# Optimization experiments

Measured on AMD Instinct MI355X. Metric: run time of the kernel, lower is better.

## Reference

```python
import jax, jax.numpy as jnp
import numpy as np
import math

SUB_LEN = 5

def _row_mask(index, sub_len, win_len):
    # Faithful port of logsparseAttention.row_mask (numpy, built at trace time).
    log_l = math.ceil(math.log2(sub_len))
    mask = np.zeros(win_len, dtype=np.float32)
    if (win_len // sub_len) * 2 * log_l > index:
        mask[: index + 1] = 1.0
    else:
        while index >= 0:
            if index - log_l + 1 < 0:
                mask[:index] = 1.0
                break
            mask[index - log_l + 1 : index + 1] = 1.0
            for i in range(log_l):
                new_index = index - log_l + 1 - 2 ** i
                if index - new_index <= sub_len and new_index >= 0:
                    mask[new_index] = 1.0
            index -= sub_len
    return mask

def _log_mask(win_len, sub_len):
    m = np.stack([_row_mask(i, sub_len, win_len) for i in range(win_len)])
    return m[None, None]  # [1, 1, L, L]

def setup_inputs() -> dict:
    key = jax.random.key(0)
    kq, kk, kv = jax.random.split(key, 3)
    B, L, H, D = 4, 2048, 16, 64
    return {
        "queries": jax.random.normal(kq, (B, L, H, D), dtype=jnp.float32),
        "keys": jax.random.normal(kk, (B, L, H, D), dtype=jnp.float32),
        "values": jax.random.normal(kv, (B, L, H, D), dtype=jnp.float32),
        "attn_mask": jnp.zeros((1,), dtype=jnp.int32),  # unused by the module
    }

def reference(queries, keys, values, attn_mask):
    L = queries.shape[1]
    mask = jnp.asarray(_log_mask(L, SUB_LEN), dtype=queries.dtype)  # [1,1,L,L]
    q = jnp.swapaxes(queries, 1, 2)            # [B, H, L, D]
    k = jnp.transpose(keys, (0, 2, 3, 1))      # [B, H, D, L]
    v = jnp.swapaxes(values, 1, 2)             # [B, H, L, D]
    pre_att = jnp.matmul(q, k)                 # [B, H, L, L] (no scaling: scale=None)
    pre_att = pre_att * mask + (-1e9) * (1.0 - mask)
    att = jax.nn.softmax(pre_att, axis=-1)
    return jnp.matmul(att, v)                  # [B, H, L, D]
```

## Files before the change

### kernel.cpp

```cpp
#include <hip/hip_runtime.h>


typedef __attribute__((ext_vector_type(8))) short short8;
typedef __attribute__((ext_vector_type(4))) float floatx4;
typedef __attribute__((ext_vector_type(16))) float floatx16;
typedef _Float16 half8 __attribute__((ext_vector_type(8)));
typedef _Float16 half4 __attribute__((ext_vector_type(4)));

#define NB 4
#define NL 2048
#define NH 16
#define ND 64
#define PADK 72
#define LOG2E 1.44269504088896340736f

#define KSW(row, col8) (((row) << 6) + ((col8) ^ (((row) & 7) << 3)))

static __device__ __forceinline__ unsigned short f2bf(float f) {
    unsigned int u = __float_as_uint(f);
    u += 0x7fff + ((u >> 16) & 1);
    return (unsigned short)(u >> 16);
}
static __device__ __forceinline__ float bf2f(unsigned short h) {
    return __uint_as_float(((unsigned int)h) << 16);
}
static __device__ __forceinline__ floatx16 fzero16() {
    floatx16 z;
    #pragma unroll
    for (int i = 0; i < 16; ++i) z[i] = 0.f;
    return z;
}

__global__ __launch_bounds__(256)
void conv_kv(const float* __restrict__ Kg, const float* __restrict__ Vg,
             _Float16* __restrict__ Kf, _Float16* __restrict__ Vt) {
    __shared__ float tile[64][65];
    const int kt = blockIdx.x;
    const int bh = blockIdx.y;
    const int b  = bh >> 4, h = bh & 15;
    const int t  = threadIdx.x;
    const int row = t >> 2;
    const int seg = (t & 3) * 16;
    const size_t gsrc = (((size_t)(b * NL + kt * 64 + row) * NH + h) << 6) + seg;
    {
        float kv[16];
        #pragma unroll
        for (int i = 0; i < 16; i += 4) *(float4*)(kv + i) = *(const float4*)(Kg + gsrc + i);
        half8 o0, o1;
        #pragma unroll
        for (int j2 = 0; j2 < 8; ++j2) {
            o0[j2] = (_Float16)(kv[j2] * LOG2E);
            o1[j2] = (_Float16)(kv[8 + j2] * LOG2E);
        }
        _Float16* kd = Kf + (((size_t)(bh * NL + kt * 64 + row)) << 6) + seg;
        *(half8*)kd = o0;
        *(half8*)(kd + 8) = o1;
    }
    {
        #pragma unroll
        for (int i = 0; i < 16; i += 4) {
            float4 v = *(const float4*)(Vg + gsrc + i);
            tile[row][seg + i + 0] = v.x;
            tile[row][seg + i + 1] = v.y;
            tile[row][seg + i + 2] = v.z;
            tile[row][seg + i + 3] = v.w;
        }
    }
    __syncthreads();
    #pragma unroll
    for (int pass = 0; pass < 2; ++pass) {
        const int d  = pass * 32 + (t >> 3);
        const int kk = (t & 7) * 8;
        half8 o;
        #pragma unroll
        for (int j2 = 0; j2 < 8; ++j2) o[j2] = (_Float16)tile[kk + j2][d];
        *(half8*)(Vt + (((size_t)(bh * 64 + d)) << 11) + kt * 64 + kk) = o;
    }
}

__global__ __launch_bounds__(256, 4)
void lsattn_main(const float* __restrict__ Qg,
                 const _Float16* __restrict__ Kf,
                 const _Float16* __restrict__ Vt,
                 float* __restrict__ Og) {
    __shared__ alignas(16) _Float16 Ks[64 * 64];
    __shared__ alignas(16) _Float16 Vs[64 * 64];
    __shared__ alignas(16) _Float16 Ps[4 * 8 * 32 * 8];

    const int id   = (int)blockIdx.x;
    const int bh   = id & 63;
    const int pr   = id >> 6;
    const int tid  = threadIdx.x;
    const int lane = tid & 63;
    const int w    = tid >> 6;
    const int wq   = w & 1;
    const int lq   = lane & 31;
    const int hi   = lane >> 5;

    const int sa   = (w < 2) ? pr : 31 - pr;
    const int qrow = sa * 64 + wq * 32 + lq;
    const int TB   = 31 - pr;

    half8 qf[4];
    {
        const float* qp = Qg + (((size_t)((bh >> 4) * NL + qrow) * NH + (bh & 15)) << 6) + hi * 8;
        #pragma unroll
        for (int c = 0; c < 4; ++c) {
            float4 a = *(const float4*)(qp + c * 16);
            float4 b = *(const float4*)(qp + c * 16 + 4);
            qf[c][0] = (_Float16)a.x; qf[c][1] = (_Float16)a.y;
            qf[c][2] = (_Float16)a.z; qf[c][3] = (_Float16)a.w;
            qf[c][4] = (_Float16)b.x; qf[c][5] = (_Float16)b.y;
            qf[c][6] = (_Float16)b.z; qf[c][7] = (_Float16)b.w;
        }
    }

    floatx16 o0 = fzero16(), o1 = fzero16();
    float m_run = -1e30f, l_run = 0.f;

    const int srow = tid >> 3;
    const int sseg = (tid & 7) * 8;
    const _Float16* kgb = Kf + ((size_t)bh * NL + srow) * 64 + sseg;
    const _Float16* vgb = Vt + ((size_t)bh << 17) + (size_t)srow * NL + sseg;
    _Float16* pbuf = Ps + w * 2048;

    half8 k0 = *(const half8*)(kgb);
    half8 k1 = *(const half8*)(kgb + 2048);
    half8 v0 = *(const half8*)(vgb);
    half8 v1 = *(const half8*)(vgb + 32 * NL);

    for (int t = 0; t <= TB; ++t) {
        __syncthreads();
        *(half8*)(Ks + KSW(srow,      sseg)) = k0;
        *(half8*)(Ks + KSW(srow + 32, sseg)) = k1;
        *(half8*)(Vs + KSW(srow,      sseg)) = v0;
        *(half8*)(Vs + KSW(srow + 32, sseg)) = v1;
        if (t < TB) {
            k0 = *(const half8*)(kgb + (size_t)(t + 1) * 4096);
            k1 = *(const half8*)(kgb + (size_t)(t + 1) * 4096 + 2048);
            v0 = *(const half8*)(vgb + (t + 1) * 64);
            v1 = *(const half8*)(vgb + (t + 1) * 64 + 32 * NL);
        }
        __syncthreads();

        if (t > sa) continue;

        const bool diag  = (t == sa);
        const bool skip1 = diag && (wq == 0);

        floatx16 s0 = fzero16(), s1;
        #pragma unroll
        for (int c = 0; c < 4; ++c) {
            half8 kf = *(const half8*)(Ks + KSW(lq, c * 16 + hi * 8));
            s0 = __builtin_amdgcn_mfma_f32_32x32x16_f16(kf, qf[c], s0, 0, 0, 0);
        }
        if (!skip1) {
            s1 = fzero16();
            #pragma unroll
            for (int c = 0; c < 4; ++c) {
                half8 kf = *(const half8*)(Ks + KSW(32 + lq, c * 16 + hi * 8));
                s1 = __builtin_amdgcn_mfma_f32_32x32x16_f16(kf, qf[c], s1, 0, 0, 0);
            }
        }

        if (diag) {
            if (wq == 0) {
                #pragma unroll
                for (int reg = 0; reg < 16; ++reg) {
                    const int key = (reg & 3) + ((reg >> 2) << 3) + (hi << 2);
                    if (key > lq) s0[reg] = -1e30f;
                }
            } else {
                #pragma unroll
                for (int reg = 0; reg < 16; ++reg) {
                    const int key = (reg & 3) + ((reg >> 2) << 3) + (hi << 2);
                    if (key > lq) s1[reg] = -1e30f;
                }
            }
        }

        float mt = s0[0];
        #pragma unroll
        for (int reg = 1; reg < 16; ++reg) mt = fmaxf(mt, s0[reg]);
        if (!skip1) {
            #pragma unroll
            for (int reg = 0; reg < 16; ++reg) mt = fmaxf(mt, s1[reg]);
        }
        mt = fmaxf(mt, __shfl_xor(mt, 32));
        if (__any(mt > m_run + 8.f)) {
            const float mn = fmaxf(m_run, mt);
            const float al = __builtin_amdgcn_exp2f(m_run - mn);
            #pragma unroll
            for (int i = 0; i < 16; ++i) { o0[i] *= al; o1[i] *= al; }
            l_run *= al;
            m_run = mn;
        }
        float ls = 0.f;
        #pragma unroll
        for (int s = 0; s < 4; ++s) {
            half4 hp;
            #pragma unroll
            for (int r = 0; r < 4; ++r) {
                const float p = __builtin_amdgcn_exp2f(s0[s * 4 + r] - m_run);
                ls += p; hp[r] = (_Float16)p;
            }
            *(half4*)(pbuf + (s * 32 + lq) * 8 + hi * 4) = hp;
        }
        if (!skip1) {
            #pragma unroll
            for (int s = 0; s < 4; ++s) {
                half4 hp;
                #pragma unroll
                for (int r = 0; r < 4; ++r) {
                    const float p = __builtin_amdgcn_exp2f(s1[s * 4 + r] - m_run);
                    ls += p; hp[r] = (_Float16)p;
                }
                *(half4*)(pbuf + ((4 + s) * 32 + lq) * 8 + hi * 4) = hp;
            }
        }
        ls += __shfl_xor(ls, 32);
        l_run += ls;

        const int cmax = skip1 ? 2 : 4;
        for (int c = 0; c < cmax; ++c) {
            half8 pf  = *(const half8*)(pbuf + ((c * 2 + hi) * 32 + lq) * 8);
            half8 vf0 = *(const half8*)(Vs + KSW(lq,      c * 16 + hi * 8));
            half8 vf1 = *(const half8*)(Vs + KSW(32 + lq, c * 16 + hi * 8));
            o0 = __builtin_amdgcn_mfma_f32_32x32x16_f16(vf0, pf, o0, 0, 0, 0);
            o1 = __builtin_amdgcn_mfma_f32_32x32x16_f16(vf1, pf, o1, 0, 0, 0);
        }
    }

    const float inv = 1.f / l_run;
    float* op = Og + ((size_t)bh * NL + qrow) * ND;
    #pragma unroll
    for (int s = 0; s < 4; ++s) {
        float4 x, y;
        x.x = o0[s * 4 + 0] * inv; x.y = o0[s * 4 + 1] * inv;
        x.z = o0[s * 4 + 2] * inv; x.w = o0[s * 4 + 3] * inv;
        *(float4*)(op + s * 8 + hi * 4) = x;
        y.x = o1[s * 4 + 0] * inv; y.y = o1[s * 4 + 1] * inv;
        y.z = o1[s * 4 + 2] * inv; y.w = o1[s * 4 + 3] * inv;
        *(float4*)(op + 32 + s * 8 + hi * 4) = y;
    }
}

__global__ __launch_bounds__(256)
void lsattn_fb(const float* __restrict__ Qg,
               const float* __restrict__ Kg,
               const float* __restrict__ Vg,
               float* __restrict__ Og) {
    __shared__ alignas(16) unsigned short Kh[64 * PADK];
    __shared__ alignas(16) unsigned short Kl[64 * PADK];
    __shared__ alignas(16) unsigned short Vh[64 * PADK];

    const int qt   = 31 - (int)blockIdx.x;
    const int bh   = blockIdx.y;
    const int tid  = threadIdx.x;
    const int lane = tid & 63;
    const int w    = tid >> 6;
    const int col  = lane & 15;
    const int quad = lane >> 4;
    const int qrow = qt * 64 + w * 16 + col;

    short8 qhi[2], qlo[2];
    {
        const float* qp = Qg + ((bh >> 4) * NL + qrow) * (NH * ND) + (bh & 15) * ND + quad * 8;
        #pragma unroll
        for (int c = 0; c < 2; ++c) {
            float qv[8];
            *(float4*)(qv + 0) = *(const float4*)(qp + c * 32);
            *(float4*)(qv + 4) = *(const float4*)(qp + c * 32 + 4);
            #pragma unroll
            for (int j = 0; j < 8; ++j) {
                unsigned short h = f2bf(qv[j]);
                qhi[c][j] = (short)h;
                qlo[c][j] = (short)f2bf(qv[j] - bf2f(h));
            }
        }
    }
    floatx4 ofrag[4];
    #pragma unroll
    for (int i = 0; i < 4; ++i) ofrag[i] = floatx4{0.f, 0.f, 0.f, 0.f};
    float m_run = -1e30f, l_run = 0.f;
    const int skey  = tid >> 2;
    const int sdb   = (tid & 3) * 16;
    const int gbase = (bh >> 4) * NL * NH * ND + (bh & 15) * ND;

    for (int t = 0; t <= qt; ++t) {
        const int j0 = t * 64;
        __syncthreads();
        {
            const int gro = gbase + (j0 + skey) * (NH * ND) + sdb;
            float kv[16], vv[16];
            #pragma unroll
            for (int i = 0; i < 16; i += 4) {
                *(float4*)(kv + i) = *(const float4*)(Kg + gro + i);
                *(float4*)(vv + i) = *(const float4*)(Vg + gro + i);
            }
            short8 h0, h1, l0, l1;
            #pragma unroll
            for (int j = 0; j < 8; ++j) {
                unsigned short h = f2bf(kv[j]);
                h0[j] = (short)h; l0[j] = (short)f2bf(kv[j] - bf2f(h));
                unsigned short g = f2bf(kv[8 + j]);
                h1[j] = (short)g; l1[j] = (short)f2bf(kv[8 + j] - bf2f(g));
            }
            *(short8*)(Kh + skey * PADK + sdb)     = h0;
            *(short8*)(Kh + skey * PADK + sdb + 8) = h1;
            *(short8*)(Kl + skey * PADK + sdb)     = l0;
            *(short8*)(Kl + skey * PADK + sdb + 8) = l1;
            #pragma unroll
            for (int i = 0; i < 16; ++i) Vh[(sdb + i) * PADK + skey] = f2bf(vv[i]);
        }
        __syncthreads();

        floatx4 stf[4];
        #pragma unroll
        for (int f = 0; f < 4; ++f) {
            floatx4 acc = floatx4{0.f, 0.f, 0.f, 0.f};
            #pragma unroll
            for (int c = 0; c < 2; ++c) {
                short8 kh = *(const short8*)(Kh + (f * 16 + col) * PADK + c * 32 + quad * 8);
                short8 kl = *(const short8*)(Kl + (f * 16 + col) * PADK + c * 32 + quad * 8);
                acc = __builtin_amdgcn_mfma_f32_16x16x32_bf16(kh, qhi[c], acc, 0, 0, 0);
                acc = __builtin_amdgcn_mfma_f32_16x16x32_bf16(kl, qhi[c], acc, 0, 0, 0);
                acc = __builtin_amdgcn_mfma_f32_16x16x32_bf16(kh, qlo[c], acc, 0, 0, 0);
            }
            stf[f] = acc;
        }
        if (t == qt) {
            #pragma unroll
            for (int f = 0; f < 4; ++f)
                #pragma unroll
                for (int r = 0; r < 4; ++r) {
                    const int key = j0 + f * 16 + quad * 4 + r;
                    if (key > qrow) stf[f][r] = -1e30f;
                }
        }
        float mt = -1e30f;
        #pragma unroll
        for (int f = 0; f < 4; ++f)
            #pragma unroll
            for (int r = 0; r < 4; ++r) mt = fmaxf(mt, stf[f][r]);
        mt = fmaxf(mt, __shfl_xor(mt, 16));
        mt = fmaxf(mt, __shfl_xor(mt, 32));
        const float m_new = fmaxf(m_run, mt);
        const float alpha = __expf(m_run - m_new);
        float ls = 0.f;
        #pragma unroll
        for (int f = 0; f < 4; ++f)
            #pragma unroll
            for (int r = 0; r < 4; ++r) {
                const float p = __expf(stf[f][r] - m_new);
                stf[f][r] = p; ls += p;
            }
        ls += __shfl_xor(ls, 16);
        ls += __shfl_xor(ls, 32);
        l_run = l_run * alpha + ls;
        m_run = m_new;
        #pragma unroll
        for (int mc = 0; mc < 4; ++mc) ofrag[mc] *= alpha;

        short8 pfrag[2];
        #pragma unroll
        for (int kc = 0; kc < 2; ++kc) {
            #pragma unroll
            for (int jj = 0; jj < 8; ++jj) {
                const int r  = jj & 3;
                const int sq = (quad & 1) * 2 + (jj >> 2);
                const int sl = col + (sq << 4);
                const float va = __shfl(stf[kc * 2 + 0][r], sl);
                const float vb = __shfl(stf[kc * 2 + 1][r], sl);
                pfrag[kc][jj] = (short)f2bf((quad & 2) ? vb : va);
            }
        }
        #pragma unroll
        for (int mc = 0; mc < 4; ++mc) {
            #pragma unroll
            for (int kc = 0; kc < 2; ++kc) {
                short8 vf = *(const short8*)(Vh + (mc * 16 + col) * PADK + kc * 32 + quad * 8);
                ofrag[mc] = __builtin_amdgcn_mfma_f32_16x16x32_bf16(vf, pfrag[kc], ofrag[mc], 0, 0, 0);
            }
        }
    }
    const float inv = 1.f / l_run;
    float* op = Og + ((size_t)bh * NL + qrow) * ND;
    #pragma unroll
    for (int mc = 0; mc < 4; ++mc) {
        float4 o;
        o.x = ofrag[mc][0] * inv; o.y = ofrag[mc][1] * inv;
        o.z = ofrag[mc][2] * inv; o.w = ofrag[mc][3] * inv;
        *(float4*)(op + mc * 16 + quad * 4) = o;
    }
}

extern "C" void kernel_launch(void* const* d_in, const int* in_sizes, int n_in,
                              void* d_out, int out_size, void* d_ws, size_t ws_size,
                              hipStream_t stream) {
    const float* Q = (const float*)d_in[0];
    const float* K = (const float*)d_in[1];
    const float* V = (const float*)d_in[2];
    float* O = (float*)d_out;

    const size_t elems = (size_t)NB * NL * NH * ND;
    if (ws_size >= 2 * elems * sizeof(_Float16)) {
        _Float16* Kf = (_Float16*)d_ws;
        _Float16* Vt = Kf + elems;
        conv_kv<<<dim3(32, 64), dim3(256), 0, stream>>>(K, V, Kf, Vt);
        lsattn_main<<<dim3(1024), dim3(256), 0, stream>>>(Q, Kf, Vt, O);
    } else {
        lsattn_fb<<<dim3(32, 64), dim3(256), 0, stream>>>(Q, K, V, O);
    }
}
```

Baseline: 187.6 us.

## Double-buffer K/V tiles and keep P in registers via permlane swaps

Double-buffers the K and V shared-memory tiles so the next tile is written while the current one is processed, leaving one barrier per iteration instead of two. It removes the shared-memory round trip for the probability matrix by packing P to fp16 in registers and redistributing it across half-waves with permlane32 swaps. It also raises wave priority around the MFMA blocks and uses tree reductions for the max and sum. In exchange it doubles the K/V shared memory, adds more live registers, and falls back to shuffles when the permlane builtin is unavailable.

Measured after the change: 201.9 us. 7.6% more time.

```diff
diff --git a/kernel.cpp b/kernel.cpp
--- a/kernel.cpp
+++ b/kernel.cpp
@@ -6,6 +6,7 @@
 typedef __attribute__((ext_vector_type(16))) float floatx16;
 typedef _Float16 half8 __attribute__((ext_vector_type(8)));
 typedef _Float16 half4 __attribute__((ext_vector_type(4)));
+typedef unsigned int uint32_t4 __attribute__((ext_vector_type(4)));
 
 #define NB 4
 #define NL 2048
@@ -29,6 +30,47 @@
     #pragma unroll
     for (int i = 0; i < 16; ++i) z[i] = 0.f;
     return z;
+}
+
+static __device__ __forceinline__ void plswap2(unsigned int& a, unsigned int& b, int hi) {
+#if __has_builtin(__builtin_amdgcn_permlane32_swap)
+    auto r = __builtin_amdgcn_permlane32_swap(a, b, false, false);
+    a = (unsigned int)r[0];
+    b = (unsigned int)r[1];
+#else
+    const unsigned int ax = (unsigned int)__shfl_xor((int)a, 32);
+    const unsigned int bx = (unsigned int)__shfl_xor((int)b, 32);
+    const unsigned int na = hi ? bx : a;
+    const unsigned int nb = hi ? b  : ax;
+    a = na; b = nb;
+#endif
+}
+static __device__ __forceinline__ float xhalf_max(float v, int hi) {
+    unsigned int a = __float_as_uint(v), b = __float_as_uint(v);
+    plswap2(a, b, hi);
+    return fmaxf(__uint_as_float(a), __uint_as_float(b));
+}
+static __device__ __forceinline__ float xhalf_sum(float v, int hi) {
+    unsigned int a = __float_as_uint(v), b = __float_as_uint(v);
+    plswap2(a, b, hi);
+    return __uint_as_float(a) + __uint_as_float(b);
+}
+
+static __device__ __forceinline__ void pack_P(const floatx16& p, int hi, half8& pfa, half8& pfb) {
+    unsigned int A0 = __builtin_bit_cast(unsigned int, __builtin_amdgcn_cvt_pkrtz(p[0],  p[1]));
+    unsigned int B0 = __builtin_bit_cast(unsigned int, __builtin_amdgcn_cvt_pkrtz(p[2],  p[3]));
+    unsigned int A1 = __builtin_bit_cast(unsigned int, __builtin_amdgcn_cvt_pkrtz(p[4],  p[5]));
+    unsigned int B1 = __builtin_bit_cast(unsigned int, __builtin_amdgcn_cvt_pkrtz(p[6],  p[7]));
+    unsigned int A2 = __builtin_bit_cast(unsigned int, __builtin_amdgcn_cvt_pkrtz(p[8],  p[9]));
+    unsigned int B2 = __builtin_bit_cast(unsigned int, __builtin_amdgcn_cvt_pkrtz(p[10], p[11]));
+    unsigned int A3 = __builtin_bit_cast(unsigned int, __builtin_amdgcn_cvt_pkrtz(p[12], p[13]));
+    unsigned int B3 = __builtin_bit_cast(unsigned int, __builtin_amdgcn_cvt_pkrtz(p[14], p[15]));
+    plswap2(A0, A1, hi); plswap2(B0, B1, hi);
+    plswap2(A2, A3, hi); plswap2(B2, B3, hi);
+    uint32_t4 wa = {A0, B0, A1, B1};
+    uint32_t4 wb = {A2, B2, A3, B3};
+    pfa = __builtin_bit_cast(half8, wa);
+    pfb = __builtin_bit_cast(half8, wb);
 }
 
 __global__ __launch_bounds__(256)
@@ -83,9 +125,8 @@
                  const _Float16* __restrict__ Kf,
                  const _Float16* __restrict__ Vt,
                  float* __restrict__ Og) {
-    __shared__ alignas(16) _Float16 Ks[64 * 64];
-    __shared__ alignas(16) _Float16 Vs[64 * 64];
-    __shared__ alignas(16) _Float16 Ps[4 * 8 * 32 * 8];
+    __shared__ alignas(16) _Float16 Ks[2][64 * 64];
+    __shared__ alignas(16) _Float16 Vs[2][64 * 64];
 
     const int id   = (int)blockIdx.x;
     const int bh   = id & 63;
@@ -122,46 +163,26 @@
     const int sseg = (tid & 7) * 8;
     const _Float16* kgb = Kf + ((size_t)bh * NL + srow) * 64 + sseg;
     const _Float16* vgb = Vt + ((size_t)bh << 17) + (size_t)srow * NL + sseg;
-    _Float16* pbuf = Ps + w * 2048;
-
-    half8 k0 = *(const half8*)(kgb);
-    half8 k1 = *(const half8*)(kgb + 2048);
-    half8 v0 = *(const half8*)(vgb);
-    half8 v1 = *(const half8*)(vgb + 32 * NL);
-
-    for (int t = 0; t <= TB; ++t) {
-        __syncthreads();
-        *(half8*)(Ks + KSW(srow,      sseg)) = k0;
-        *(half8*)(Ks + KSW(srow + 32, sseg)) = k1;
-        *(half8*)(Vs + KSW(srow,      sseg)) = v0;
-        *(half8*)(Vs + KSW(srow + 32, sseg)) = v1;
-        if (t < TB) {
-            k0 = *(const half8*)(kgb + (size_t)(t + 1) * 4096);
-            k1 = *(const half8*)(kgb + (size_t)(t + 1) * 4096 + 2048);
-            v0 = *(const half8*)(vgb + (t + 1) * 64);
-            v1 = *(const half8*)(vgb + (t + 1) * 64 + 32 * NL);
-        }
-        __syncthreads();
-
-        if (t > sa) continue;
-
+
+    auto process_tile = [&](int t, const _Float16* Ksb, const _Float16* Vsb) {
         const bool diag  = (t == sa);
         const bool skip1 = diag && (wq == 0);
 
-        floatx16 s0 = fzero16(), s1;
+        floatx16 s0 = fzero16(), s1 = fzero16();
+        __builtin_amdgcn_s_setprio(1);
         #pragma unroll
         for (int c = 0; c < 4; ++c) {
-            half8 kf = *(const half8*)(Ks + KSW(lq, c * 16 + hi * 8));
+            half8 kf = *(const half8*)(Ksb + KSW(lq, c * 16 + hi * 8));
             s0 = __builtin_amdgcn_mfma_f32_32x32x16_f16(kf, qf[c], s0, 0, 0, 0);
         }
         if (!skip1) {
-            s1 = fzero16();
             #pragma unroll
             for (int c = 0; c < 4; ++c) {
-                half8 kf = *(const half8*)(Ks + KSW(32 + lq, c * 16 + hi * 8));
+                half8 kf = *(const half8*)(Ksb + KSW(32 + lq, c * 16 + hi * 8));
                 s1 = __builtin_amdgcn_mfma_f32_32x32x16_f16(kf, qf[c], s1, 0, 0, 0);
             }
         }
+        __builtin_amdgcn_s_setprio(0);
 
         if (diag) {
             if (wq == 0) {
@@ -179,14 +200,20 @@
             }
         }
 
-        float mt = s0[0];
-        #pragma unroll
-        for (int reg = 1; reg < 16; ++reg) mt = fmaxf(mt, s0[reg]);
+        float m4[4];
+        #pragma unroll
+        for (int s = 0; s < 4; ++s)
+            m4[s] = fmaxf(fmaxf(s0[4*s], s0[4*s+1]), fmaxf(s0[4*s+2], s0[4*s+3]));
+        float mt = fmaxf(fmaxf(m4[0], m4[1]), fmaxf(m4[2], m4[3]));
         if (!skip1) {
-            #pragma unroll
-            for (int reg = 0; reg < 16; ++reg) mt = fmaxf(mt, s1[reg]);
-        }
-        mt = fmaxf(mt, __shfl_xor(mt, 32));
+            float n4[4];
+            #pragma unroll
+            for (int s = 0; s < 4; ++s)
+                n4[s] = fmaxf(fmaxf(s1[4*s], s1[4*s+1]), fmaxf(s1[4*s+2], s1[4*s+3]));
+            mt = fmaxf(mt, fmaxf(fmaxf(n4[0], n4[1]), fmaxf(n4[2], n4[3])));
+        }
+        mt = xhalf_max(mt, hi);
+
         if (__any(mt > m_run + 8.f)) {
             const float mn = fmaxf(m_run, mt);
             const float al = __builtin_amdgcn_exp2f(m_run - mn);
@@ -195,40 +222,88 @@
             l_run *= al;
             m_run = mn;
         }
-        float ls = 0.f;
-        #pragma unroll
-        for (int s = 0; s < 4; ++s) {
-            half4 hp;
-            #pragma unroll
-            for (int r = 0; r < 4; ++r) {
-                const float p = __builtin_amdgcn_exp2f(s0[s * 4 + r] - m_run);
-                ls += p; hp[r] = (_Float16)p;
-            }
-            *(half4*)(pbuf + (s * 32 + lq) * 8 + hi * 4) = hp;
-        }
+
+        floatx16 p0;
+        #pragma unroll
+        for (int i = 0; i < 16; ++i) p0[i] = __builtin_amdgcn_exp2f(s0[i] - m_run);
+        float t4[4];
+        #pragma unroll
+        for (int s = 0; s < 4; ++s)
+            t4[s] = (p0[4*s] + p0[4*s+1]) + (p0[4*s+2] + p0[4*s+3]);
+        float ls = (t4[0] + t4[1]) + (t4[2] + t4[3]);
+
+        half8 pf0, pf1, pf2, pf3;
+        pack_P(p0, hi, pf0, pf1);
         if (!skip1) {
-            #pragma unroll
-            for (int s = 0; s < 4; ++s) {
-                half4 hp;
-                #pragma unroll
-                for (int r = 0; r < 4; ++r) {
-                    const float p = __builtin_amdgcn_exp2f(s1[s * 4 + r] - m_run);
-                    ls += p; hp[r] = (_Float16)p;
-                }
-                *(half4*)(pbuf + ((4 + s) * 32 + lq) * 8 + hi * 4) = hp;
-            }
-        }
-        ls += __shfl_xor(ls, 32);
-        l_run += ls;
-
-        const int cmax = skip1 ? 2 : 4;
-        for (int c = 0; c < cmax; ++c) {
-            half8 pf  = *(const half8*)(pbuf + ((c * 2 + hi) * 32 + lq) * 8);
-            half8 vf0 = *(const half8*)(Vs + KSW(lq,      c * 16 + hi * 8));
-            half8 vf1 = *(const half8*)(Vs + KSW(32 + lq, c * 16 + hi * 8));
+            floatx16 p1;
+            #pragma unroll
+            for (int i = 0; i < 16; ++i) p1[i] = __builtin_amdgcn_exp2f(s1[i] - m_run);
+            float u4[4];
+            #pragma unroll
+            for (int s = 0; s < 4; ++s)
+                u4[s] = (p1[4*s] + p1[4*s+1]) + (p1[4*s+2] + p1[4*s+3]);
+            ls += (u4[0] + u4[1]) + (u4[2] + u4[3]);
+            pack_P(p1, hi, pf2, pf3);
+        }
+        l_run += xhalf_sum(ls, hi);
+
+        __builtin_amdgcn_s_setprio(1);
+        #pragma unroll
+        for (int c = 0; c < 2; ++c) {
+            half8 pf  = (c == 0) ? pf0 : pf1;
+            half8 vf0 = *(const half8*)(Vsb + KSW(lq,      c * 16 + hi * 8));
+            half8 vf1 = *(const half8*)(Vsb + KSW(32 + lq, c * 16 + hi * 8));
             o0 = __builtin_amdgcn_mfma_f32_32x32x16_f16(vf0, pf, o0, 0, 0, 0);
             o1 = __builtin_amdgcn_mfma_f32_32x32x16_f16(vf1, pf, o1, 0, 0, 0);
         }
+        if (!skip1) {
+            #pragma unroll
+            for (int c = 2; c < 4; ++c) {
+                half8 pf  = (c == 2) ? pf2 : pf3;
+                half8 vf0 = *(const half8*)(Vsb + KSW(lq,      c * 16 + hi * 8));
+                half8 vf1 = *(const half8*)(Vsb + KSW(32 + lq, c * 16 + hi * 8));
+                o0 = __builtin_amdgcn_mfma_f32_32x32x16_f16(vf0, pf, o0, 0, 0, 0);
+                o1 = __builtin_amdgcn_mfma_f32_32x32x16_f16(vf1, pf, o1, 0, 0, 0);
+            }
+        }
+        __builtin_amdgcn_s_setprio(0);
+    };
+
+    {
+        half8 k0 = *(const half8*)(kgb);
+        half8 k1 = *(const half8*)(kgb + 2048);
+        half8 v0 = *(const half8*)(vgb);
+        half8 v1 = *(const half8*)(vgb + 32 * NL);
+        *(half8*)(Ks[0] + KSW(srow,      sseg)) = k0;
+        *(half8*)(Ks[0] + KSW(srow + 32, sseg)) = k1;
+        *(half8*)(Vs[0] + KSW(srow,      sseg)) = v0;
+        *(half8*)(Vs[0] + KSW(srow + 32, sseg)) = v1;
+    }
+    half8 k0 = *(const half8*)(kgb + 4096);
+    half8 k1 = *(const half8*)(kgb + 4096 + 2048);
+    half8 v0 = *(const half8*)(vgb + 64);
+    half8 v1 = *(const half8*)(vgb + 64 + 32 * NL);
+    __syncthreads();
+
+    int cur = 0;
+    for (int t = 0; t <= TB; ++t) {
+        if (t < TB) {
+            _Float16* kd = Ks[cur ^ 1];
+            _Float16* vd = Vs[cur ^ 1];
+            *(half8*)(kd + KSW(srow,      sseg)) = k0;
+            *(half8*)(kd + KSW(srow + 32, sseg)) = k1;
+            *(half8*)(vd + KSW(srow,      sseg)) = v0;
+            *(half8*)(vd + KSW(srow + 32, sseg)) = v1;
+            if (t + 1 < TB) {
+                k0 = *(const half8*)(kgb + (size_t)(t + 2) * 4096);
+                k1 = *(const half8*)(kgb + (size_t)(t + 2) * 4096 + 2048);
+                v0 = *(const half8*)(vgb + (t + 2) * 64);
+                v1 = *(const half8*)(vgb + (t + 2) * 64 + 32 * NL);
+            }
+        }
+        if (t <= sa) process_tile(t, Ks[cur], Vs[cur]);
+        if (t < TB) __syncthreads();
+        cur ^= 1;
     }
 
     const float inv = 1.f / l_run;
```
